# Kernel optimization log

Measured on AMD Instinct MI355X. Metric: run time of the kernel, lower is better.

The kernel has to match this reference:

```python
import jax, jax.numpy as jnp
import numpy as np

B, S, D, H = 2, 2048, 1024, 16
DEPTH = D // H


def setup_inputs() -> dict:
    key = jax.random.key(0)
    ks = jax.random.split(key, 10)
    std = 1.0 / np.sqrt(D)
    v = jax.random.normal(ks[0], (B, S, D), jnp.float32)
    q = jax.random.normal(ks[1], (B, S, D), jnp.float32)
    k = jax.random.normal(ks[2], (B, S, D), jnp.float32)
    # padding mask: 1.0 at masked (padded) key positions, 0.0 elsewhere
    mask = (jax.random.uniform(ks[3], (B, 1, 1, S)) < 0.1).astype(jnp.float32)
    Wq = jax.random.normal(ks[4], (D, D), jnp.float32) * std
    bq = jnp.zeros((D,), jnp.float32)
    Wv = jax.random.normal(ks[5], (D, D), jnp.float32) * std
    bv = jnp.zeros((D,), jnp.float32)
    Wo = jax.random.normal(ks[6], (D, D), jnp.float32) * std
    bo = jnp.zeros((D,), jnp.float32)
    return {"v": v, "q": q, "k": k, "mask": mask,
            "Wq": Wq, "bq": bq, "Wv": Wv, "bv": bv, "Wo": Wo, "bo": bo}


def _split_heads(x):
    # (B, S, D) -> (B, H, S, depth)
    return x.reshape(B, S, H, DEPTH).transpose(0, 2, 1, 3)


def reference(v, q, k, mask, Wq, bq, Wv, bv, Wo, bo):
    # NOTE: faithful to source, keys are projected with the QUERY weights
    # (mixedK = self.wQuery(k) in the original code).
    Q = _split_heads(q @ Wq + bq)
    K = _split_heads(k @ Wq + bq)
    V = _split_heads(v @ Wv + bv)
    scale = 1.0 / jnp.sqrt(jnp.asarray(DEPTH, jnp.float32))
    logits = jnp.einsum('bhqd,bhkd->bhqk', Q, K) * scale
    logits = logits + mask * (-1e9)
    attn = jax.nn.softmax(logits, axis=-1)
    out = jnp.einsum('bhqk,bhkd->bhqd', attn, V)
    out = out.transpose(0, 2, 1, 3).reshape(B, S, D)
    return out @ Wo + bo
```

## Files before the change

kernel.cpp:

```cpp
#include <hip/hip_runtime.h>
#include <cstddef>


namespace {

constexpr int Ss = 2048;
constexpr int Dd = 1024;
constexpr int Mm = 4096;
constexpr int NT = Ss / 64;
constexpr float QSCALE = 0.18033688f;
constexpr float NEG2 = -1.442695041e9f;

typedef unsigned short u16;
typedef __attribute__((ext_vector_type(8))) __bf16 bf16x8;
typedef __attribute__((ext_vector_type(4))) float f32x4;
typedef __attribute__((ext_vector_type(16))) float f32x16;
typedef __attribute__((ext_vector_type(4))) unsigned int u32x4;
typedef __attribute__((ext_vector_type(2))) unsigned int u32x2;
typedef __attribute__((ext_vector_type(8))) unsigned short us8;

__device__ __forceinline__ u16 bfc(float f) {
  __bf16 h = (__bf16)f;
  return __builtin_bit_cast(u16, h);
}
__device__ __forceinline__ unsigned pack2(float lo, float hi) {
  return (unsigned)bfc(lo) | ((unsigned)bfc(hi) << 16);
}

__device__ __forceinline__ void gload_lds16(const void* g, void* l) {
  __builtin_amdgcn_global_load_lds(
      (__attribute__((address_space(1))) void*)g,
      (__attribute__((address_space(3))) void*)l, 16, 0, 0);
}

__device__ __forceinline__ f32x4 mfma16(bf16x8 a, bf16x8 b, f32x4 c) {
  return __builtin_amdgcn_mfma_f32_16x16x32_bf16(a, b, c, 0, 0, 0);
}
__device__ __forceinline__ f32x16 mfma32(bf16x8 a, bf16x8 b, f32x16 c) {
  return __builtin_amdgcn_mfma_f32_32x32x16_bf16(a, b, c, 0, 0, 0);
}
__device__ __forceinline__ float exp2_fast(float x) {
  return __builtin_amdgcn_exp2f(x);
}

__device__ __forceinline__ void pl32swap(unsigned& a, unsigned& b) {
#if __has_builtin(__builtin_amdgcn_permlane32_swap)
  u32x2 r = __builtin_amdgcn_permlane32_swap(a, b, false, false);
  a = r[0];
  b = r[1];
#else
  unsigned ax = (unsigned)__shfl_xor((int)a, 32);
  unsigned bx = (unsigned)__shfl_xor((int)b, 32);
  bool hi = (threadIdx.x & 63) >= 32;
  unsigned na = hi ? bx : a;
  unsigned nb = hi ? b : ax;
  a = na;
  b = nb;
#endif
}

#define PIPE_BARRIER_V(N)                                  \
  do {                                                     \
    asm volatile("s_waitcnt vmcnt(" #N ")" ::: "memory");  \
    __builtin_amdgcn_sched_barrier(0);                     \
    __builtin_amdgcn_s_barrier();                          \
    __builtin_amdgcn_sched_barrier(0);                     \
  } while (0)

__device__ __forceinline__ int swz(int row, int col) {
  return row * 64 + ((((col >> 3) ^ (row & 7)) << 3) | (col & 7));
}
__device__ __forceinline__ int src_col(int lane) {
  return ((lane & 7) ^ (lane >> 3)) * 8;
}

__global__ __launch_bounds__(256) void wt_transpose(const float* __restrict__ W0,
                                                    const float* __restrict__ W1,
                                                    const float* __restrict__ W2,
                                                    u16* __restrict__ wsbase) {
  const float* W = (blockIdx.z == 0) ? W0 : (blockIdx.z == 1) ? W1 : W2;
  u16* WT = wsbase + (size_t)blockIdx.z * (1024 * 1024);
  __shared__ float tile[32][33];
  const int tid = threadIdx.x;
  const int tx = tid & 31;
  const int ty = tid >> 5;
  const int n0 = blockIdx.x * 32;
  const int k0 = blockIdx.y * 32;
#pragma unroll
  for (int i = 0; i < 4; ++i)
    tile[ty + i * 8][tx] = W[(size_t)(k0 + ty + i * 8) * 1024 + n0 + tx];
  __syncthreads();
  const int r = tid >> 3;
  const int c4 = (tid & 7) * 4;
  ushort4 o4 = make_ushort4(bfc(tile[c4 + 0][r]), bfc(tile[c4 + 1][r]),
                            bfc(tile[c4 + 2][r]), bfc(tile[c4 + 3][r]));
  *(ushort4*)(&WT[(size_t)(n0 + r) * 1024 + k0 + c4]) = o4;
}

__global__ __launch_bounds__(256) void cvt_bf16(const float* __restrict__ q,
                                                const float* __restrict__ k,
                                                const float* __restrict__ v,
                                                u16* __restrict__ qb,
                                                u16* __restrict__ kb,
                                                u16* __restrict__ vb) {
  const int which = (int)(blockIdx.x >> 11);
  const int blk = (int)(blockIdx.x & 2047);
  const float* src = (which == 0) ? q : (which == 1) ? k : v;
  u16* dst = (which == 0) ? qb : (which == 1) ? kb : vb;
  const int base = (blk * 256 + (int)threadIdx.x) * 8;
  const float4 a = *(const float4*)(src + base);
  const float4 b = *(const float4*)(src + base + 4);
  us8 o;
  o[0] = bfc(a.x); o[1] = bfc(a.y); o[2] = bfc(a.z); o[3] = bfc(a.w);
  o[4] = bfc(b.x); o[5] = bfc(b.y); o[6] = bfc(b.z); o[7] = bfc(b.w);
  *(us8*)(dst + base) = o;
}

__global__ __launch_bounds__(256) void proj_qkv(
    const u16* __restrict__ qb, const u16* __restrict__ kb,
    const u16* __restrict__ vb, const u16* __restrict__ WqT,
    const u16* __restrict__ WvT, const float* __restrict__ bq,
    const float* __restrict__ bv, u16* __restrict__ Qp, u16* __restrict__ Kp,
    u16* __restrict__ VpT) {
  constexpr int K = 1024, N = 1024, M = 4096;
  __shared__ u16 As[128 * 64];
  __shared__ u16 Bs[128 * 64];
  const int lin = (int)blockIdx.x;
  const int xcd = lin & 7;
  const int j = lin >> 3;
  const int panel = xcd * 12 + (j >> 3);
  const int ntile = j & 7;
  const int z = panel >> 5;
  const int mtile = panel & 31;
  const int n0 = ntile * 128;
  const int m0 = mtile * 128;

  const u16* A = (z == 0) ? qb : (z == 1) ? kb : vb;
  const u16* Bt = (z == 2) ? WvT : WqT;
  const float* bias = (z == 2) ? bv : bq;
  const float cscale = (z == 0) ? QSCALE : 1.0f;

  const int tid = threadIdx.x;
  const int wid = tid >> 6;
  const int lane = tid & 63;
  const int g = lane >> 4;
  const int lr = lane & 15;
  const int wr = wid >> 1, wc = wid & 1;

  const f32x4 zero = {0.f, 0.f, 0.f, 0.f};
  f32x4 acc[4][4];
#pragma unroll
  for (int m = 0; m < 4; ++m)
#pragma unroll
    for (int n = 0; n < 4; ++n) acc[m][n] = zero;

  for (int kt = 0; kt < 16; ++kt) {
#pragma unroll
    for (int jj = 0; jj < 4; ++jj) {
      int rb = (wid * 4 + jj) * 8;
      gload_lds16(&A[(size_t)(m0 + rb + (lane >> 3)) * K + kt * 64 + src_col(lane)],
                  &As[rb * 64]);
      gload_lds16(&Bt[(size_t)(n0 + rb + (lane >> 3)) * K + kt * 64 + src_col(lane)],
                  &Bs[rb * 64]);
    }
    __syncthreads();
#pragma unroll
    for (int kk = 0; kk < 2; ++kk) {
      bf16x8 a[4], b[4];
#pragma unroll
      for (int m = 0; m < 4; ++m)
        a[m] = *(const bf16x8*)(&As[swz(wr * 64 + m * 16 + lr, kk * 32 + g * 8)]);
#pragma unroll
      for (int n = 0; n < 4; ++n)
        b[n] = *(const bf16x8*)(&Bs[swz(wc * 64 + n * 16 + lr, kk * 32 + g * 8)]);
#pragma unroll
      for (int m = 0; m < 4; ++m)
#pragma unroll
        for (int n = 0; n < 4; ++n) acc[m][n] = mfma16(a[m], b[n], acc[m][n]);
    }
    __syncthreads();
  }

#pragma unroll
  for (int n = 0; n < 4; ++n) {
    const int col = n0 + wc * 64 + n * 16 + lr;
    const float bv_ = bias[col];
#pragma unroll
    for (int m = 0; m < 4; ++m) {
      const int rowb = m0 + wr * 64 + m * 16 + g * 4;
      if (z == 2) {
        ushort4 o4 = make_ushort4(bfc(acc[m][n][0] + bv_), bfc(acc[m][n][1] + bv_),
                                  bfc(acc[m][n][2] + bv_), bfc(acc[m][n][3] + bv_));
        *(ushort4*)(&VpT[(size_t)col * M + rowb]) = o4;
      } else {
        u16* Cp = (z == 0) ? Qp : Kp;
#pragma unroll
        for (int r = 0; r < 4; ++r)
          Cp[(size_t)(rowb + r) * N + col] = bfc((acc[m][n][r] + bv_) * cscale);
      }
    }
  }
}

__global__ __launch_bounds__(256) void gemm_o(const u16* __restrict__ Ap,
                                              const u16* __restrict__ Bt,
                                              const float* __restrict__ bias,
                                              float* __restrict__ Cp) {
  constexpr int K = 1024, N = 1024;
  __shared__ u16 As[3][128 * 64];
  __shared__ u16 Bs[3][64 * 64];
  const int lin = (int)blockIdx.x;
  const int xcd = lin & 7;
  const int j = lin >> 3;
  const int mtile = xcd * 4 + (j >> 4);
  const int ntile = j & 15;
  const int n0 = ntile * 64;
  const int m0 = mtile * 128;

  const int tid = threadIdx.x;
  const int wid = tid >> 6;
  const int lane = tid & 63;
  const int g = lane >> 4;
  const int lr = lane & 15;

  const f32x4 zero = {0.f, 0.f, 0.f, 0.f};
  f32x4 acc[2][4];
#pragma unroll
  for (int m = 0; m < 2; ++m)
#pragma unroll
    for (int n = 0; n < 4; ++n) acc[m][n] = zero;

  auto stage = [&](int kt, u16* as, u16* bs) {
#pragma unroll
    for (int jj = 0; jj < 4; ++jj) {
      int rb = (wid * 4 + jj) * 8;
      gload_lds16(&Ap[(size_t)(m0 + rb + (lane >> 3)) * K + kt * 64 + src_col(lane)],
                  as + rb * 64);
    }
#pragma unroll
    for (int jj = 0; jj < 2; ++jj) {
      int rb = (wid * 2 + jj) * 8;
      gload_lds16(&Bt[(size_t)(n0 + rb + (lane >> 3)) * K + kt * 64 + src_col(lane)],
                  bs + rb * 64);
    }
  };

  stage(0, As[0], Bs[0]);
  stage(1, As[1], Bs[1]);

  int b0 = 0;
  for (int kt = 0; kt < 16; ++kt) {
    if (kt < 15) PIPE_BARRIER_V(6);
    else         PIPE_BARRIER_V(0);
    if (kt + 2 < 16) {
      int b2 = b0 + 2; if (b2 >= 3) b2 -= 3;
      stage(kt + 2, As[b2], Bs[b2]);
    }
    const u16* as = As[b0];
    const u16* bs = Bs[b0];
#pragma unroll
    for (int kk = 0; kk < 2; ++kk) {
      bf16x8 a[2], b[4];
#pragma unroll
      for (int m = 0; m < 2; ++m)
        a[m] = *(const bf16x8*)(&as[swz(wid * 32 + m * 16 + lr, kk * 32 + g * 8)]);
#pragma unroll
      for (int n = 0; n < 4; ++n)
        b[n] = *(const bf16x8*)(&bs[swz(n * 16 + lr, kk * 32 + g * 8)]);
#pragma unroll
      for (int m = 0; m < 2; ++m)
#pragma unroll
        for (int n = 0; n < 4; ++n) acc[m][n] = mfma16(a[m], b[n], acc[m][n]);
    }
    b0 = (b0 == 2) ? 0 : b0 + 1;
  }
#pragma unroll
  for (int n = 0; n < 4; ++n) {
    const int col = n0 + n * 16 + lr;
    const float bv_ = bias[col];
#pragma unroll
    for (int m = 0; m < 2; ++m) {
      const int rowb = m0 + wid * 32 + m * 16 + g * 4;
#pragma unroll
      for (int r = 0; r < 4; ++r)
        Cp[(size_t)(rowb + r) * N + col] = acc[m][n][r] + bv_;
    }
  }
}

__global__ __launch_bounds__(256) void attn32(const u16* __restrict__ Qp,
                                              const u16* __restrict__ Kp,
                                              const u16* __restrict__ VpT,
                                              const float* __restrict__ mask,
                                              u16* __restrict__ Op) {
  __shared__ u16 Ks[3][64 * 64];
  __shared__ u16 Vt[3][64 * 64];
  __shared__ float msall[Ss];
  const int tid = threadIdx.x;
  const int wid = tid >> 6;
  const int lane = tid & 63;
  const int l31 = lane & 31;
  const int hi = lane >> 5;
  const int lin = (int)(blockIdx.x + (blockIdx.y << 4));
  const int wl = (lin & 7) * 64 + (lin >> 3);
  const int qt = wl & 15;
  const int bh = wl >> 4;
  const int b = bh >> 4;
  const int h = bh & 15;
  const int q0 = qt * 128;
  const size_t base = ((size_t)b * Ss) * Dd + (size_t)h * 64;
  const size_t vbase = (size_t)h * 64 * Mm + (size_t)b * Ss;
  const int qrow = q0 + wid * 32 + l31;

  auto stageKV = [&](int t, u16* ksb, u16* vtb) {
    const int key0 = t * 64;
#pragma unroll
    for (int jj = 0; jj < 2; ++jj) {
      int rb = (wid * 2 + jj) * 8;
      gload_lds16(&Kp[base + (size_t)(key0 + rb + (lane >> 3)) * Dd + src_col(lane)],
                  ksb + rb * 64);
      gload_lds16(&VpT[vbase + (size_t)(rb + (lane >> 3)) * Mm + key0 + src_col(lane)],
                  vtb + rb * 64);
    }
  };

  bf16x8 qf[4];
#pragma unroll
  for (int ks = 0; ks < 4; ++ks)
    qf[ks] = *(const bf16x8*)(&Qp[base + (size_t)qrow * Dd + ks * 16 + hi * 8]);
  const float4 mk0 = *(const float4*)(&mask[(size_t)b * Ss + tid * 8]);
  const float4 mk1 = *(const float4*)(&mask[(size_t)b * Ss + tid * 8 + 4]);

  stageKV(0, Ks[0], Vt[0]);
  stageKV(1, Ks[1], Vt[1]);

  {
    f32x4 s0 = {mk0.x * NEG2, mk0.y * NEG2, mk0.z * NEG2, mk0.w * NEG2};
    f32x4 s1 = {mk1.x * NEG2, mk1.y * NEG2, mk1.z * NEG2, mk1.w * NEG2};
    *(f32x4*)(&msall[tid * 8]) = s0;
    *(f32x4*)(&msall[tid * 8 + 4]) = s1;
  }
  asm volatile("s_waitcnt lgkmcnt(0)" ::: "memory");
  __builtin_amdgcn_sched_barrier(0);
  __builtin_amdgcn_s_barrier();
  __builtin_amdgcn_sched_barrier(0);

  f32x16 oacc[2], lacc;
#pragma unroll
  for (int i = 0; i < 2; ++i)
#pragma unroll
    for (int r = 0; r < 16; ++r) oacc[i][r] = 0.f;
#pragma unroll
  for (int r = 0; r < 16; ++r) lacc[r] = 0.f;

  bf16x8 vones;
  {
    us8 o;
#pragma unroll
    for (int i = 0; i < 8; ++i) o[i] = 0x3F80;
    vones = __builtin_bit_cast(bf16x8, o);
  }

  int b0 = 0;
  for (int t = 0; t < NT; ++t) {
    if (t < NT - 1) PIPE_BARRIER_V(4);
    else            PIPE_BARRIER_V(0);
    if (t + 2 < NT) {
      int b2 = b0 + 2; if (b2 >= 3) b2 -= 3;
      stageKV(t + 2, Ks[b2], Vt[b2]);
    }
    const u16* ks = Ks[b0];
    const u16* vt = Vt[b0];
    const float* msp = &msall[t * 64];

    f32x16 sacc[2];
#pragma unroll
    for (int sub = 0; sub < 2; ++sub)
#pragma unroll
      for (int a = 0; a < 4; ++a)
        *(f32x4*)((float*)&sacc[sub] + a * 4) =
            *(const f32x4*)(&msp[sub * 32 + a * 8 + hi * 4]);
    __builtin_amdgcn_s_setprio(1);
#pragma unroll
    for (int sub = 0; sub < 2; ++sub)
#pragma unroll
      for (int ks_ = 0; ks_ < 4; ++ks_) {
        bf16x8 kf =
            *(const bf16x8*)(&ks[swz(sub * 32 + l31, ks_ * 16 + hi * 8)]);
        sacc[sub] = mfma32(kf, qf[ks_], sacc[sub]);
      }
    __builtin_amdgcn_s_setprio(0);

#pragma unroll
    for (int sub = 0; sub < 2; ++sub)
#pragma unroll
      for (int r = 0; r < 16; ++r) sacc[sub][r] = exp2_fast(sacc[sub][r]);

    bf16x8 pa[4];
#pragma unroll
    for (int sub = 0; sub < 2; ++sub)
#pragma unroll
      for (int half = 0; half < 2; ++half) {
        const int bse = half * 8;
        unsigned A0 = pack2(sacc[sub][bse + 0], sacc[sub][bse + 1]);
        unsigned A1 = pack2(sacc[sub][bse + 2], sacc[sub][bse + 3]);
        unsigned B0 = pack2(sacc[sub][bse + 4], sacc[sub][bse + 5]);
        unsigned B1 = pack2(sacc[sub][bse + 6], sacc[sub][bse + 7]);
        pl32swap(A0, B0);
        pl32swap(A1, B1);
        u32x4 w = {A0, A1, B0, B1};
        pa[sub * 2 + half] = __builtin_bit_cast(bf16x8, w);
      }

    __builtin_amdgcn_s_setprio(1);
#pragma unroll
    for (int dsub = 0; dsub < 2; ++dsub)
#pragma unroll
      for (int ks_ = 0; ks_ < 4; ++ks_) {
        bf16x8 vf =
            *(const bf16x8*)(&vt[swz(dsub * 32 + l31, ks_ * 16 + hi * 8)]);
        oacc[dsub] = mfma32(pa[ks_], vf, oacc[dsub]);
      }
#pragma unroll
    for (int ks_ = 0; ks_ < 4; ++ks_)
      lacc = mfma32(pa[ks_], vones, lacc);
    __builtin_amdgcn_s_setprio(0);

    b0 = (b0 == 2) ? 0 : b0 + 1;
  }

  float rl[16];
#pragma unroll
  for (int r = 0; r < 16; ++r) rl[r] = __builtin_amdgcn_rcpf(lacc[r]);
#pragma unroll
  for (int dsub = 0; dsub < 2; ++dsub) {
    const int col = h * 64 + dsub * 32 + l31;
#pragma unroll
    for (int r = 0; r < 16; ++r) {
      const int row = q0 + wid * 32 + (r & 3) + 8 * (r >> 2) + 4 * hi;
      Op[((size_t)b * Ss + row) * Dd + col] = bfc(oacc[dsub][r] * rl[r]);
    }
  }
}

}

extern "C" void kernel_launch(void* const* d_in, const int* in_sizes, int n_in,
                              void* d_out, int out_size, void* d_ws, size_t ws_size,
                              hipStream_t stream) {
  (void)in_sizes; (void)n_in; (void)out_size; (void)ws_size;
  const float* v = (const float*)d_in[0];
  const float* q = (const float*)d_in[1];
  const float* k = (const float*)d_in[2];
  const float* mask = (const float*)d_in[3];
  const float* Wq = (const float*)d_in[4];
  const float* bq = (const float*)d_in[5];
  const float* Wv = (const float*)d_in[6];
  const float* bv = (const float*)d_in[7];
  const float* Wo = (const float*)d_in[8];
  const float* bo = (const float*)d_in[9];
  float* out = (float*)d_out;

  constexpr size_t MEG = 1024 * 1024;
  u16* ws = (u16*)d_ws;
  u16* WqT = ws;
  u16* WvT = ws + 1 * MEG;
  u16* WoT = ws + 2 * MEG;
  u16* qb  = ws + 3 * MEG;
  u16* kb  = ws + 7 * MEG;
  u16* vb  = ws + 11 * MEG;
  u16* Qp  = ws + 15 * MEG;
  u16* Kp  = ws + 19 * MEG;
  u16* VpT = ws + 23 * MEG;
  u16* AO  = qb;

  wt_transpose<<<dim3(32, 32, 3), 256, 0, stream>>>(Wq, Wv, Wo, ws);
  cvt_bf16<<<dim3(6144), 256, 0, stream>>>(q, k, v, qb, kb, vb);
  proj_qkv<<<dim3(768), 256, 0, stream>>>(qb, kb, vb, WqT, WvT, bq, bv, Qp, Kp, VpT);
  attn32<<<dim3(16, 32), 256, 0, stream>>>(Qp, Kp, VpT, mask, AO);
  gemm_o<<<dim3(512), 256, 0, stream>>>(AO, WoT, bo, out);
}
```

Baseline: 135.4 us.

## Split attention key tiles across warps and fold padding mask into V

The attention kernel now uses 64-query blocks, twice as many as before. Two warp pairs split each 64-key tile between them, and their partial O and row-sum accumulators are combined through LDS at the end. The additive mask on the logits is replaced: the V projection writes zeros at masked key rows, and the row sum is taken with an MFMA against a per-key valid vector instead of all-ones. This removes the mask loads and adds from the inner loop and doubles grid parallelism. The cost is an extra reduction through shared memory and duplicated K/V staging across blocks.

```diff
diff --git a/kernel.cpp b/kernel.cpp
--- a/kernel.cpp
+++ b/kernel.cpp
@@ -9,7 +9,6 @@
 constexpr int Mm = 4096;
 constexpr int NT = Ss / 64;
 constexpr float QSCALE = 0.18033688f;
-constexpr float NEG2 = -1.442695041e9f;
 
 typedef unsigned short u16;
 typedef __attribute__((ext_vector_type(8))) __bf16 bf16x8;
@@ -120,8 +119,8 @@
     const u16* __restrict__ qb, const u16* __restrict__ kb,
     const u16* __restrict__ vb, const u16* __restrict__ WqT,
     const u16* __restrict__ WvT, const float* __restrict__ bq,
-    const float* __restrict__ bv, u16* __restrict__ Qp, u16* __restrict__ Kp,
-    u16* __restrict__ VpT) {
+    const float* __restrict__ bv, const float* __restrict__ maskf,
+    u16* __restrict__ Qp, u16* __restrict__ Kp, u16* __restrict__ VpT) {
   constexpr int K = 1024, N = 1024, M = 4096;
   __shared__ u16 As[128 * 64];
   __shared__ u16 Bs[128 * 64];
@@ -189,8 +188,12 @@
     for (int m = 0; m < 4; ++m) {
       const int rowb = m0 + wr * 64 + m * 16 + g * 4;
       if (z == 2) {
-        ushort4 o4 = make_ushort4(bfc(acc[m][n][0] + bv_), bfc(acc[m][n][1] + bv_),
-                                  bfc(acc[m][n][2] + bv_), bfc(acc[m][n][3] + bv_));
+        const f32x4 mk = *(const f32x4*)(&maskf[rowb]);
+        ushort4 o4;
+        o4.x = (mk[0] != 0.f) ? (u16)0 : bfc(acc[m][n][0] + bv_);
+        o4.y = (mk[1] != 0.f) ? (u16)0 : bfc(acc[m][n][1] + bv_);
+        o4.z = (mk[2] != 0.f) ? (u16)0 : bfc(acc[m][n][2] + bv_);
+        o4.w = (mk[3] != 0.f) ? (u16)0 : bfc(acc[m][n][3] + bv_);
         *(ushort4*)(&VpT[(size_t)col * M + rowb]) = o4;
       } else {
         u16* Cp = (z == 0) ? Qp : Kp;
@@ -295,22 +298,24 @@
                                               u16* __restrict__ Op) {
   __shared__ u16 Ks[3][64 * 64];
   __shared__ u16 Vt[3][64 * 64];
-  __shared__ float msall[Ss];
+  __shared__ u16 validall[Ss];
   const int tid = threadIdx.x;
   const int wid = tid >> 6;
   const int lane = tid & 63;
   const int l31 = lane & 31;
   const int hi = lane >> 5;
-  const int lin = (int)(blockIdx.x + (blockIdx.y << 4));
-  const int wl = (lin & 7) * 64 + (lin >> 3);
-  const int qt = wl & 15;
-  const int bh = wl >> 4;
+  const int qhalf = wid & 1;
+  const int kh = wid >> 1;
+  const int lin = (int)(blockIdx.x + (blockIdx.y << 5));
+  const int wl = (lin & 7) * 128 + (lin >> 3);
+  const int qt = wl & 31;
+  const int bh = wl >> 5;
   const int b = bh >> 4;
   const int h = bh & 15;
-  const int q0 = qt * 128;
+  const int q0 = qt * 64;
   const size_t base = ((size_t)b * Ss) * Dd + (size_t)h * 64;
   const size_t vbase = (size_t)h * 64 * Mm + (size_t)b * Ss;
-  const int qrow = q0 + wid * 32 + l31;
+  const int qrow = q0 + qhalf * 32 + l31;
 
   auto stageKV = [&](int t, u16* ksb, u16* vtb) {
     const int key0 = t * 64;
@@ -335,31 +340,31 @@
   stageKV(1, Ks[1], Vt[1]);
 
   {
-    f32x4 s0 = {mk0.x * NEG2, mk0.y * NEG2, mk0.z * NEG2, mk0.w * NEG2};
-    f32x4 s1 = {mk1.x * NEG2, mk1.y * NEG2, mk1.z * NEG2, mk1.w * NEG2};
-    *(f32x4*)(&msall[tid * 8]) = s0;
-    *(f32x4*)(&msall[tid * 8 + 4]) = s1;
+    us8 vv;
+    vv[0] = (mk0.x != 0.f) ? (u16)0 : (u16)0x3F80;
+    vv[1] = (mk0.y != 0.f) ? (u16)0 : (u16)0x3F80;
+    vv[2] = (mk0.z != 0.f) ? (u16)0 : (u16)0x3F80;
+    vv[3] = (mk0.w != 0.f) ? (u16)0 : (u16)0x3F80;
+    vv[4] = (mk1.x != 0.f) ? (u16)0 : (u16)0x3F80;
+    vv[5] = (mk1.y != 0.f) ? (u16)0 : (u16)0x3F80;
+    vv[6] = (mk1.z != 0.f) ? (u16)0 : (u16)0x3F80;
+    vv[7] = (mk1.w != 0.f) ? (u16)0 : (u16)0x3F80;
+    *(us8*)(&validall[tid * 8]) = vv;
   }
   asm volatile("s_waitcnt lgkmcnt(0)" ::: "memory");
   __builtin_amdgcn_sched_barrier(0);
   __builtin_amdgcn_s_barrier();
   __builtin_amdgcn_sched_barrier(0);
 
-  f32x16 oacc[2], lacc;
+  f32x16 oacc[2], lacc, zero16;
+#pragma unroll
+  for (int r = 0; r < 16; ++r) zero16[r] = 0.f;
 #pragma unroll
   for (int i = 0; i < 2; ++i)
 #pragma unroll
     for (int r = 0; r < 16; ++r) oacc[i][r] = 0.f;
 #pragma unroll
   for (int r = 0; r < 16; ++r) lacc[r] = 0.f;
-
-  bf16x8 vones;
-  {
-    us8 o;
-#pragma unroll
-    for (int i = 0; i < 8; ++i) o[i] = 0x3F80;
-    vones = __builtin_bit_cast(bf16x8, o);
-  }
 
   int b0 = 0;
   for (int t = 0; t < NT; ++t) {
@@ -371,74 +376,87 @@
     }
     const u16* ks = Ks[b0];
     const u16* vt = Vt[b0];
-    const float* msp = &msall[t * 64];
-
-    f32x16 sacc[2];
-#pragma unroll
-    for (int sub = 0; sub < 2; ++sub)
-#pragma unroll
-      for (int a = 0; a < 4; ++a)
-        *(f32x4*)((float*)&sacc[sub] + a * 4) =
-            *(const f32x4*)(&msp[sub * 32 + a * 8 + hi * 4]);
+
+    f32x16 sacc;
+    {
+      bf16x8 kf = *(const bf16x8*)(&ks[swz(kh * 32 + l31, 0 * 16 + hi * 8)]);
+      sacc = mfma32(kf, qf[0], zero16);
+    }
     __builtin_amdgcn_s_setprio(1);
 #pragma unroll
-    for (int sub = 0; sub < 2; ++sub)
-#pragma unroll
-      for (int ks_ = 0; ks_ < 4; ++ks_) {
-        bf16x8 kf =
-            *(const bf16x8*)(&ks[swz(sub * 32 + l31, ks_ * 16 + hi * 8)]);
-        sacc[sub] = mfma32(kf, qf[ks_], sacc[sub]);
+    for (int ks_ = 1; ks_ < 4; ++ks_) {
+      bf16x8 kf = *(const bf16x8*)(&ks[swz(kh * 32 + l31, ks_ * 16 + hi * 8)]);
+      sacc = mfma32(kf, qf[ks_], sacc);
+    }
+    __builtin_amdgcn_s_setprio(0);
+
+#pragma unroll
+    for (int r = 0; r < 16; ++r) sacc[r] = exp2_fast(sacc[r]);
+
+    bf16x8 pa[2];
+#pragma unroll
+    for (int slot = 0; slot < 2; ++slot) {
+      const int bse = slot * 8;
+      unsigned A0 = pack2(sacc[bse + 0], sacc[bse + 1]);
+      unsigned A1 = pack2(sacc[bse + 2], sacc[bse + 3]);
+      unsigned B0 = pack2(sacc[bse + 4], sacc[bse + 5]);
+      unsigned B1 = pack2(sacc[bse + 6], sacc[bse + 7]);
+      pl32swap(A0, B0);
+      pl32swap(A1, B1);
+      u32x4 w = {A0, A1, B0, B1};
+      pa[slot] = __builtin_bit_cast(bf16x8, w);
+    }
+
+    __builtin_amdgcn_s_setprio(1);
+#pragma unroll
+    for (int slot = 0; slot < 2; ++slot) {
+      const int kbase = t * 64 + kh * 32 + slot * 16 + hi * 8;
+      bf16x8 vd = *(const bf16x8*)(&validall[kbase]);
+#pragma unroll
+      for (int dsub = 0; dsub < 2; ++dsub) {
+        bf16x8 vf = *(const bf16x8*)(
+            &vt[swz(dsub * 32 + l31, kh * 32 + slot * 16 + hi * 8)]);
+        oacc[dsub] = mfma32(pa[slot], vf, oacc[dsub]);
       }
+      lacc = mfma32(pa[slot], vd, lacc);
+    }
     __builtin_amdgcn_s_setprio(0);
 
-#pragma unroll
-    for (int sub = 0; sub < 2; ++sub)
-#pragma unroll
-      for (int r = 0; r < 16; ++r) sacc[sub][r] = exp2_fast(sacc[sub][r]);
-
-    bf16x8 pa[4];
-#pragma unroll
-    for (int sub = 0; sub < 2; ++sub)
-#pragma unroll
-      for (int half = 0; half < 2; ++half) {
-        const int bse = half * 8;
-        unsigned A0 = pack2(sacc[sub][bse + 0], sacc[sub][bse + 1]);
-        unsigned A1 = pack2(sacc[sub][bse + 2], sacc[sub][bse + 3]);
-        unsigned B0 = pack2(sacc[sub][bse + 4], sacc[sub][bse + 5]);
-        unsigned B1 = pack2(sacc[sub][bse + 6], sacc[sub][bse + 7]);
-        pl32swap(A0, B0);
-        pl32swap(A1, B1);
-        u32x4 w = {A0, A1, B0, B1};
-        pa[sub * 2 + half] = __builtin_bit_cast(bf16x8, w);
+    b0 = (b0 == 2) ? 0 : b0 + 1;
+  }
+
+  __syncthreads();
+  float* rbuf = (float*)(&Ks[0][0]);
+  if (kh == 1) {
+    float* p = rbuf + qhalf * 3072 + lane;
+#pragma unroll
+    for (int r = 0; r < 16; ++r) p[r * 64] = oacc[0][r];
+#pragma unroll
+    for (int r = 0; r < 16; ++r) p[(16 + r) * 64] = oacc[1][r];
+#pragma unroll
+    for (int r = 0; r < 16; ++r) p[(32 + r) * 64] = lacc[r];
+  }
+  __syncthreads();
+  if (kh == 0) {
+    const float* p = rbuf + qhalf * 3072 + lane;
+#pragma unroll
+    for (int r = 0; r < 16; ++r) oacc[0][r] += p[r * 64];
+#pragma unroll
+    for (int r = 0; r < 16; ++r) oacc[1][r] += p[(16 + r) * 64];
+#pragma unroll
+    for (int r = 0; r < 16; ++r) lacc[r] += p[(32 + r) * 64];
+
+    float rl[16];
+#pragma unroll
+    for (int r = 0; r < 16; ++r) rl[r] = __builtin_amdgcn_rcpf(lacc[r]);
+#pragma unroll
+    for (int dsub = 0; dsub < 2; ++dsub) {
+      const int col = h * 64 + dsub * 32 + l31;
+#pragma unroll
+      for (int r = 0; r < 16; ++r) {
+        const int row = q0 + qhalf * 32 + (r & 3) + 8 * (r >> 2) + 4 * hi;
+        Op[((size_t)b * Ss + row) * Dd + col] = bfc(oacc[dsub][r] * rl[r]);
       }
-
-    __builtin_amdgcn_s_setprio(1);
-#pragma unroll
-    for (int dsub = 0; dsub < 2; ++dsub)
-#pragma unroll
-      for (int ks_ = 0; ks_ < 4; ++ks_) {
-        bf16x8 vf =
-            *(const bf16x8*)(&vt[swz(dsub * 32 + l31, ks_ * 16 + hi * 8)]);
-        oacc[dsub] = mfma32(pa[ks_], vf, oacc[dsub]);
-      }
-#pragma unroll
-    for (int ks_ = 0; ks_ < 4; ++ks_)
-      lacc = mfma32(pa[ks_], vones, lacc);
-    __builtin_amdgcn_s_setprio(0);
-
-    b0 = (b0 == 2) ? 0 : b0 + 1;
-  }
-
-  float rl[16];
-#pragma unroll
-  for (int r = 0; r < 16; ++r) rl[r] = __builtin_amdgcn_rcpf(lacc[r]);
-#pragma unroll
-  for (int dsub = 0; dsub < 2; ++dsub) {
-    const int col = h * 64 + dsub * 32 + l31;
-#pragma unroll
-    for (int r = 0; r < 16; ++r) {
-      const int row = q0 + wid * 32 + (r & 3) + 8 * (r >> 2) + 4 * hi;
-      Op[((size_t)b * Ss + row) * Dd + col] = bfc(oacc[dsub][r] * rl[r]);
     }
   }
 }
@@ -476,7 +494,8 @@
 
   wt_transpose<<<dim3(32, 32, 3), 256, 0, stream>>>(Wq, Wv, Wo, ws);
   cvt_bf16<<<dim3(6144), 256, 0, stream>>>(q, k, v, qb, kb, vb);
-  proj_qkv<<<dim3(768), 256, 0, stream>>>(qb, kb, vb, WqT, WvT, bq, bv, Qp, Kp, VpT);
-  attn32<<<dim3(16, 32), 256, 0, stream>>>(Qp, Kp, VpT, mask, AO);
+  proj_qkv<<<dim3(768), 256, 0, stream>>>(qb, kb, vb, WqT, WvT, bq, bv, mask,
+                                          Qp, Kp, VpT);
+  attn32<<<dim3(32, 32), 256, 0, stream>>>(Qp, Kp, VpT, mask, AO);
   gemm_o<<<dim3(512), 256, 0, stream>>>(AO, WoT, bo, out);
 }
```

After: 152.1 us. +12.4%, slower.
